# Kernel optimization log

Measured on AMD Instinct MI355X. Metric: run time of the kernel, lower is better.

## Reference

```python
import jax, jax.numpy as jnp
import numpy as np

NUM_HEADS = 8
NUM_GROUPS = 32  # min(C//4, 32) for C=512
EPS = 1e-6       # flax GroupNorm default


def setup_inputs() -> dict:
    key = jax.random.key(0)
    ks = jax.random.split(key, 3)
    B, H, W, D, C = 2, 16, 16, 16, 512
    x = jax.random.normal(ks[0], (B, H, W, D, C), dtype=jnp.float32)
    w_qkv = jax.random.normal(ks[1], (C, 3 * C), dtype=jnp.float32) / np.sqrt(C)
    w_proj = jax.random.normal(ks[2], (C, C), dtype=jnp.float32) / np.sqrt(C)
    return {
        "x": x,
        "gn_scale": jnp.ones((C,), jnp.float32),
        "gn_bias": jnp.zeros((C,), jnp.float32),
        "w_qkv": w_qkv,
        "b_qkv": jnp.zeros((3 * C,), jnp.float32),
        "w_proj": w_proj,
        "b_proj": jnp.zeros((C,), jnp.float32),
    }


def group_norm(x, scale, bias):
    # x: [B, S, C]; normalize within each of NUM_GROUPS channel groups over (S, group-channels)
    B, S, C = x.shape
    xg = x.reshape(B, S, NUM_GROUPS, C // NUM_GROUPS)
    mean = jnp.mean(xg, axis=(1, 3), keepdims=True)
    var = jnp.var(xg, axis=(1, 3), keepdims=True)
    xn = (xg - mean) * jax.lax.rsqrt(var + EPS)
    return xn.reshape(B, S, C) * scale + bias


def reference(x, gn_scale, gn_bias, w_qkv, b_qkv, w_proj, b_proj):
    B, H, W, D, C = x.shape
    S = H * W * D
    hd = C // NUM_HEADS
    xf = x.reshape(B, S, C)
    q_in = group_norm(xf, gn_scale, gn_bias)
    # 1x1x1 conv == per-position dense
    qkv = q_in @ w_qkv + b_qkv                      # [B, S, 3C]
    qkv = qkv.reshape(B, S, NUM_HEADS, 3 * hd)
    q, k, v = jnp.split(qkv, 3, axis=-1)            # each [B, S, nh, hd]
    scale = 1.0 / jnp.sqrt(jnp.asarray(hd, x.dtype))
    logits = jnp.einsum('btnh,bfnh->bnft', k, q * scale)  # [B, nh, S, S]
    weights = jax.nn.softmax(logits, axis=-1)
    h = jnp.einsum('bnft,btnh->bfnh', weights, v)   # [B, S, nh, hd]
    h = h.reshape(B, S, C) @ w_proj + b_proj
    return h.reshape(x.shape) + x
```

## Files before the change

kernel.cpp:

```cpp
#include <hip/hip_runtime.h>

typedef __attribute__((ext_vector_type(8))) short short8;
typedef __attribute__((ext_vector_type(4))) float f32x4;
typedef __attribute__((ext_vector_type(16))) float f32x16;

#define S_LEN 4096
#define C_DIM 512
#define NH 8
#define HD 64
#define NG 32
#define GS 16
#define LOG2E 1.44269504088896340736f

__device__ __forceinline__ unsigned short f2bf(float f) {
  union { float f; unsigned int u; } v; v.f = f;
  unsigned int r = v.u + 0x7fffu + ((v.u >> 16) & 1u);
  return (unsigned short)(r >> 16);
}

__device__ __forceinline__ float bf2f(unsigned short s) {
  union { unsigned u; float f; } v; v.u = (unsigned)s << 16;
  return v.f;
}

__device__ __forceinline__ float fexp2(float x) {
  float r;
  asm("v_exp_f32 %0, %1" : "=v"(r) : "v"(x));
  return r;
}

__device__ __forceinline__ unsigned pk_bf16(float a, float b) {
  unsigned r;
  asm("v_cvt_pk_bf16_f32 %0, %1, %2" : "=v"(r) : "v"(a), "v"(b));
  return r;
}

__device__ __forceinline__ void pl_swap(unsigned& a, unsigned& b) {
  asm("v_permlane32_swap_b32 %0, %1" : "+v"(a), "+v"(b));
}

__device__ __forceinline__ void gload_lds16(const void* g, void* l) {
  __builtin_amdgcn_global_load_lds((const __attribute__((address_space(1))) void*)g,
                                   (__attribute__((address_space(3))) void*)l, 16, 0, 0);
}

__global__ __launch_bounds__(256) void prep_kernel(const float* __restrict__ x,
                                                   float* __restrict__ partials,
                                                   const float* __restrict__ w_qkv,
                                                   unsigned short* __restrict__ wqkvT,
                                                   const float* __restrict__ w_proj,
                                                   unsigned short* __restrict__ wprojT) {
  __shared__ float tile[32][33];
  __shared__ float r1[4], r2[4];
  int bid = blockIdx.x;
  if (bid < 256) {
    int bg = bid >> 2, chunk = bid & 3;
    int b = bg >> 5, g = bg & 31;
    const float* xp = x + (size_t)b * S_LEN * C_DIM + g * GS;
    float s1 = 0.f, s2 = 0.f;
    for (int i = threadIdx.x; i < 1024 * 4; i += 256) {
      int s = chunk * 1024 + (i >> 2), c4 = i & 3;
      float4 v = *(const float4*)&xp[(size_t)s * C_DIM + c4 * 4];
      s1 += v.x + v.y + v.z + v.w;
      s2 += v.x * v.x + v.y * v.y + v.z * v.z + v.w * v.w;
    }
    for (int off = 1; off < 64; off <<= 1) {
      s1 += __shfl_xor(s1, off);
      s2 += __shfl_xor(s2, off);
    }
    int w = threadIdx.x >> 6;
    if ((threadIdx.x & 63) == 0) { r1[w] = s1; r2[w] = s2; }
    __syncthreads();
    if (threadIdx.x == 0) {
      partials[bg * 8 + chunk * 2]     = r1[0] + r1[1] + r1[2] + r1[3];
      partials[bg * 8 + chunk * 2 + 1] = r2[0] + r2[1] + r2[2] + r2[3];
    }
    return;
  }
  const float* src; unsigned short* dst; int K, N, n0, k0;
  if (bid < 1024) {
    int t = bid - 256;  src = w_qkv;  dst = wqkvT;  K = 512; N = 1536;
    n0 = (t % 48) * 32; k0 = (t / 48) * 32;
  } else {
    int t = bid - 1024; src = w_proj; dst = wprojT; K = 512; N = 512;
    n0 = (t % 16) * 32; k0 = (t / 16) * 32;
  }
  int c = threadIdx.x & 31, r0 = threadIdx.x >> 5;
  for (int i = 0; i < 4; ++i) {
    int r = r0 + i * 8;
    tile[r][c] = src[(size_t)(k0 + r) * N + n0 + c];
  }
  __syncthreads();
  for (int i = 0; i < 4; ++i) {
    int r = r0 + i * 8;
    dst[(size_t)(n0 + r) * K + k0 + c] = f2bf(tile[c][r]);
  }
}

__global__ __launch_bounds__(256) void gn_apply_kernel(const float* __restrict__ x,
                                                       const float* __restrict__ partials,
                                                       const float* __restrict__ scale,
                                                       const float* __restrict__ bias,
                                                       unsigned short* __restrict__ out) {
  int idx = blockIdx.x * 256 + threadIdx.x;
  int e = idx * 4;
  int c = e & (C_DIM - 1);
  int bs = e >> 9;
  int b = bs >> 12;
  int grp = b * NG + (c >> 4);
  float s1 = partials[grp * 8] + partials[grp * 8 + 2] + partials[grp * 8 + 4] + partials[grp * 8 + 6];
  float s2 = partials[grp * 8 + 1] + partials[grp * 8 + 3] + partials[grp * 8 + 5] + partials[grp * 8 + 7];
  const float invN = 1.0f / (float)(S_LEN * GS);
  float mean = s1 * invN;
  float var = s2 * invN - mean * mean;
  float rstd = rsqrtf(var + 1e-6f);
  float4 v = *(const float4*)&x[e];
  ushort4 o;
  o.x = f2bf((v.x - mean) * rstd * scale[c]     + bias[c]);
  o.y = f2bf((v.y - mean) * rstd * scale[c + 1] + bias[c + 1]);
  o.z = f2bf((v.z - mean) * rstd * scale[c + 2] + bias[c + 2]);
  o.w = f2bf((v.w - mean) * rstd * scale[c + 3] + bias[c + 3]);
  *(ushort4*)&out[e] = o;
}

template <int MODE>
__global__ __launch_bounds__(256) void gemm_kernel(const unsigned short* __restrict__ A,
                                                   const unsigned short* __restrict__ Bt,
                                                   const float* __restrict__ bias,
                                                   unsigned short* __restrict__ qh,
                                                   unsigned short* __restrict__ kh,
                                                   unsigned short* __restrict__ vh,
                                                   const float* __restrict__ resid,
                                                   float* __restrict__ outf) {
  __shared__ unsigned char Alds[16384];
  __shared__ unsigned char Blds[16384];
  int tid = threadIdx.x, lane = tid & 63, w = tid >> 6;
  int li = lane & 15, g = lane >> 4;
  int wr = (w >> 1) * 64, wc = (w & 1) * 64;
  int m0 = blockIdx.y * 128, n0 = blockIdx.x * 128;

  int srow = tid >> 3;
  int colS = (tid & 7) * 16;
  int sc   = colS ^ ((srow & 7) << 4);
  const char* aSrc = (const char*)A + (size_t)(m0 + srow) * 1024 + sc;
  const char* bSrc = (const char*)Bt + (size_t)(n0 + srow) * 1024 + sc;

  f32x4 acc[4][4];
  for (int i = 0; i < 4; ++i)
    for (int j = 0; j < 4; ++j) acc[i][j] = (f32x4){0.f, 0.f, 0.f, 0.f};

  for (int k0 = 0; k0 < 512; k0 += 64) {
#pragma unroll
    for (int r = 0; r < 4; ++r) {
      gload_lds16(aSrc + (size_t)r * 32 * 1024 + k0 * 2, &Alds[r * 4096 + tid * 16]);
      gload_lds16(bSrc + (size_t)r * 32 * 1024 + k0 * 2, &Blds[r * 4096 + tid * 16]);
    }
    asm volatile("s_waitcnt vmcnt(0)" ::: "memory");
    __builtin_amdgcn_s_barrier();

#pragma unroll
    for (int ks = 0; ks < 2; ++ks) {
      short8 af[4], bfm[4];
#pragma unroll
      for (int mi = 0; mi < 4; ++mi) {
        int row = wr + mi * 16 + li;
        af[mi] = *(const short8*)&Alds[row * 128 + ((ks * 64 + g * 16) ^ ((row & 7) << 4))];
      }
#pragma unroll
      for (int ni = 0; ni < 4; ++ni) {
        int row = wc + ni * 16 + li;
        bfm[ni] = *(const short8*)&Blds[row * 128 + ((ks * 64 + g * 16) ^ ((row & 7) << 4))];
      }
#pragma unroll
      for (int mi = 0; mi < 4; ++mi)
#pragma unroll
        for (int ni = 0; ni < 4; ++ni)
          acc[mi][ni] = __builtin_amdgcn_mfma_f32_16x16x32_bf16(af[mi], bfm[ni], acc[mi][ni], 0, 0, 0);
    }
    __syncthreads();
  }

  if (MODE == 0) {
    for (int ni = 0; ni < 4; ++ni) {
      int n = n0 + wc + ni * 16 + li;
      float bn = bias[n];
      int head = n / 192;
      int rem = n - head * 192;
      int part = rem >> 6;
      int h = rem & 63;
      unsigned short* dst = part == 0 ? qh : (part == 1 ? kh : vh);
      float mul = part == 0 ? 0.125f * LOG2E : 1.0f;
      for (int mi = 0; mi < 4; ++mi)
        for (int j = 0; j < 4; ++j) {
          int m = m0 + wr + mi * 16 + g * 4 + j;
          int b = m >> 12, s = m & 4095;
          float val = (acc[mi][ni][j] + bn) * mul;
          size_t idx;
          if (part == 2) idx = ((size_t)(b * NH + head) * HD + h) * S_LEN + s;
          else           idx = ((size_t)(b * NH + head) * S_LEN + s) * HD + h;
          dst[idx] = f2bf(val);
        }
    }
  } else {
    for (int ni = 0; ni < 4; ++ni) {
      int n = n0 + wc + ni * 16 + li;
      float bn = bias[n];
      for (int mi = 0; mi < 4; ++mi)
        for (int j = 0; j < 4; ++j) {
          int m = m0 + wr + mi * 16 + g * 4 + j;
          size_t off = (size_t)m * C_DIM + n;
          outf[off] = acc[mi][ni][j] + bn + resid[off];
        }
    }
  }
}

template <int SPLIT>
__global__ __launch_bounds__(256, 4) void attn_kernel(const unsigned short* __restrict__ qh,
                                                      const unsigned short* __restrict__ kh,
                                                      const unsigned short* __restrict__ vt,
                                                      unsigned short* __restrict__ ob,
                                                      unsigned short* __restrict__ opart,
                                                      float* __restrict__ lpart) {
  __shared__ unsigned char Kt[3 * 4096];
  __shared__ unsigned char Vt[3 * 4096];
  int bn = blockIdx.y;
  int half = SPLIT > 1 ? blockIdx.z : 0;
  int tid = threadIdx.x, lane = tid & 63, wv = tid >> 6;
  int r32 = lane & 31, hi_ = lane >> 5;
  int q0 = blockIdx.x * 128 + wv * 32;
  const int NT = S_LEN / 32 / SPLIT;
  const unsigned short* qp = qh + (size_t)bn * S_LEN * HD;
  const char* kp = (const char*)(kh + (size_t)bn * S_LEN * HD);
  const char* vp = (const char*)(vt + (size_t)bn * HD * S_LEN);

  int srow  = wv * 8 + (lane >> 3);
  int scolS = (lane & 7) * 16;
  int sc    = scolS ^ ((srow & 7) << 4);
  const char* kSrc = kp + (size_t)srow * 128 + sc + (size_t)half * (S_LEN / SPLIT) * 128;
  int vh_ = srow + ((sc >> 6) << 5);
  const char* vSrc = vp + (size_t)vh_ * (S_LEN * 2) + (sc & 63) + (size_t)half * (S_LEN / SPLIT) * 2;

  short8 qf[4];
#pragma unroll
  for (int ks = 0; ks < 4; ++ks)
    qf[ks] = *(const short8*)&qp[(size_t)(q0 + r32) * HD + ks * 16 + hi_ * 8];

  union { unsigned u[4]; short8 v; } ones;
#pragma unroll
  for (int i = 0; i < 4; ++i) ones.u[i] = 0x3F803F80u;

  f32x16 o0, o1, lacc, z16;
#pragma unroll
  for (int i = 0; i < 16; ++i) { o0[i] = 0.f; o1[i] = 0.f; lacc[i] = 0.f; z16[i] = 0.f; }

  int swzr = (r32 & 7) << 4;
  int sBase = wv * 1024;

  gload_lds16(kSrc, &Kt[sBase]);
  gload_lds16(vSrc, &Vt[sBase]);
  gload_lds16(kSrc + 32 * 128, &Kt[4096 + sBase]);
  gload_lds16(vSrc + 32 * 2,   &Vt[4096 + sBase]);
  asm volatile("s_waitcnt vmcnt(2)" ::: "memory");
  __builtin_amdgcn_s_barrier();

  int curO = 0, nxtO = 4096, nnO = 8192;
  for (int it = 0; it < NT; ++it) {
    bool more = (it + 2 < NT);
    if (more) {
      size_t t0n = (size_t)(it + 2) * 32;
      gload_lds16(kSrc + t0n * 128, &Kt[nnO + sBase]);
      gload_lds16(vSrc + t0n * 2,   &Vt[nnO + sBase]);
    }

    const unsigned char* Kr = &Kt[curO + r32 * 128];
    const unsigned char* Vr = &Vt[curO + r32 * 128];
    short8 kf[4], vf[4];
#pragma unroll
    for (int ks = 0; ks < 4; ++ks)
      kf[ks] = *(const short8*)&Kr[(ks * 32 + hi_ * 16) ^ swzr];
#pragma unroll
    for (int kk = 0; kk < 2; ++kk)
#pragma unroll
      for (int hf = 0; hf < 2; ++hf)
        vf[kk * 2 + hf] = *(const short8*)&Vr[(hf * 64 + kk * 32 + hi_ * 16) ^ swzr];

    f32x16 s = __builtin_amdgcn_mfma_f32_32x32x16_bf16(kf[0], qf[0], z16, 0, 0, 0);
#pragma unroll
    for (int ks = 1; ks < 4; ++ks)
      s = __builtin_amdgcn_mfma_f32_32x32x16_bf16(kf[ks], qf[ks], s, 0, 0, 0);

#pragma unroll
    for (int i = 0; i < 16; ++i) s[i] = fexp2(s[i]);

    unsigned pkv[8];
#pragma unroll
    for (int g2 = 0; g2 < 8; ++g2) pkv[g2] = pk_bf16(s[2 * g2], s[2 * g2 + 1]);
    pl_swap(pkv[0], pkv[2]); pl_swap(pkv[1], pkv[3]);
    pl_swap(pkv[4], pkv[6]); pl_swap(pkv[5], pkv[7]);
    union { unsigned u[4]; short8 v; } F0, F1;
    F0.u[0] = pkv[0]; F0.u[1] = pkv[1]; F0.u[2] = pkv[2]; F0.u[3] = pkv[3];
    F1.u[0] = pkv[4]; F1.u[1] = pkv[5]; F1.u[2] = pkv[6]; F1.u[3] = pkv[7];

    o0 = __builtin_amdgcn_mfma_f32_32x32x16_bf16(vf[0], F0.v, o0, 0, 0, 0);
    o1 = __builtin_amdgcn_mfma_f32_32x32x16_bf16(vf[1], F0.v, o1, 0, 0, 0);
    lacc = __builtin_amdgcn_mfma_f32_32x32x16_bf16(ones.v, F0.v, lacc, 0, 0, 0);
    o0 = __builtin_amdgcn_mfma_f32_32x32x16_bf16(vf[2], F1.v, o0, 0, 0, 0);
    o1 = __builtin_amdgcn_mfma_f32_32x32x16_bf16(vf[3], F1.v, o1, 0, 0, 0);
    lacc = __builtin_amdgcn_mfma_f32_32x32x16_bf16(ones.v, F1.v, lacc, 0, 0, 0);

    if (more) asm volatile("s_waitcnt vmcnt(2)" ::: "memory");
    else      asm volatile("s_waitcnt vmcnt(0)" ::: "memory");
    __builtin_amdgcn_s_barrier();
    int t = curO; curO = nxtO; nxtO = nnO; nnO = t;
  }

  if (SPLIT == 1) {
    float inv = 1.0f / lacc[0];
    int b = bn >> 3, n = bn & 7;
    size_t base = ((size_t)(b * S_LEN + q0 + r32)) * C_DIM + n * HD;
#pragma unroll
    for (int r = 0; r < 16; ++r) {
      int hrow = (r & 3) + 8 * (r >> 2) + 4 * hi_;
      ob[base + hrow]      = f2bf(o0[r] * inv);
      ob[base + 32 + hrow] = f2bf(o1[r] * inv);
    }
  } else {
    size_t row = (size_t)(bn * SPLIT + half) * S_LEN + q0 + r32;
    unsigned short* pp = opart + row * 64;
#pragma unroll
    for (int i = 0; i < 8; ++i) {
      int r = 2 * i;
      int hrow = (r & 3) + 8 * (r >> 2) + 4 * hi_;
      *(unsigned*)&pp[hrow]      = pk_bf16(o0[r], o0[r + 1]);
      *(unsigned*)&pp[32 + hrow] = pk_bf16(o1[r], o1[r + 1]);
    }
    if (!hi_) lpart[row] = lacc[0];
  }
}

template <int SPLIT>
__global__ __launch_bounds__(256) void attn_combine_kernel(const unsigned short* __restrict__ opart,
                                                           const float* __restrict__ lpart,
                                                           unsigned short* __restrict__ ob) {
  int idx = blockIdx.x * 256 + threadIdx.x;
  int h0 = (idx & 7) * 8;
  int q  = (idx >> 3) & (S_LEN - 1);
  int bn = idx >> 15;
  float acc[8];
#pragma unroll
  for (int j = 0; j < 8; ++j) acc[j] = 0.f;
  float lsum = 0.f;
#pragma unroll
  for (int z = 0; z < SPLIT; ++z) {
    size_t row = (size_t)(bn * SPLIT + z) * S_LEN + q;
    lsum += lpart[row];
    short8 a = *(const short8*)&opart[row * 64 + h0];
#pragma unroll
    for (int j = 0; j < 8; ++j) acc[j] += bf2f((unsigned short)a[j]);
  }
  float inv = 1.0f / lsum;
  union { unsigned short us[8]; short8 v; } R;
#pragma unroll
  for (int j = 0; j < 8; ++j) R.us[j] = f2bf(acc[j] * inv);
  int b_ = bn >> 3, n = bn & 7;
  *(short8*)&ob[((size_t)(b_ * S_LEN + q)) * C_DIM + n * HD + h0] = R.v;
}

extern "C" void kernel_launch(void* const* d_in, const int* in_sizes, int n_in,
                              void* d_out, int out_size, void* d_ws, size_t ws_size,
                              hipStream_t stream) {
  const float* x        = (const float*)d_in[0];
  const float* gn_scale = (const float*)d_in[1];
  const float* gn_bias  = (const float*)d_in[2];
  const float* w_qkv    = (const float*)d_in[3];
  const float* b_qkv    = (const float*)d_in[4];
  const float* w_proj   = (const float*)d_in[5];
  const float* b_proj   = (const float*)d_in[6];
  float* out = (float*)d_out;

  char* ws = (char*)d_ws;
  unsigned short* q_in   = (unsigned short*)(ws);
  unsigned short* wqkvT  = (unsigned short*)(ws + 8388608);
  unsigned short* wprojT = (unsigned short*)(ws + 9961472);
  unsigned short* qhb    = (unsigned short*)(ws + 10485760);
  unsigned short* khb    = (unsigned short*)(ws + 18874368);
  unsigned short* vtb    = (unsigned short*)(ws + 27262976);
  unsigned short* ahb    = (unsigned short*)(ws + 35651584);
  float* partials        = (float*)(ws + 44040192);
  float* lpart           = (float*)(ws + 44042240);
  unsigned short* opart  = (unsigned short*)(ws + 45090816);
  const size_t NEED2 = 45090816ull + (size_t)16 * 2 * S_LEN * 64 * 2;

  prep_kernel<<<1280, 256, 0, stream>>>(x, partials, w_qkv, wqkvT, w_proj, wprojT);
  gn_apply_kernel<<<4096, 256, 0, stream>>>(x, partials, gn_scale, gn_bias, q_in);
  gemm_kernel<0><<<dim3(12, 64), 256, 0, stream>>>(q_in, wqkvT, b_qkv, qhb, khb, vtb, nullptr, nullptr);
  if (ws_size >= NEED2) {
    attn_kernel<2><<<dim3(32, 16, 2), 256, 0, stream>>>(qhb, khb, vtb, ahb, opart, lpart);
    attn_combine_kernel<2><<<2048, 256, 0, stream>>>(opart, lpart, ahb);
  } else {
    attn_kernel<1><<<dim3(32, 16, 1), 256, 0, stream>>>(qhb, khb, vtb, ahb, nullptr, nullptr);
  }
  gemm_kernel<1><<<dim3(4, 64), 256, 0, stream>>>(ahb, wprojT, b_proj, nullptr, nullptr, nullptr, x, out);
}
```

Measured before the change: 153.5 us.

## Fuse split-KV attention combine into output projection GEMM; vectorize V stores

Removes the separate attention-combine kernel. The output projection GEMM now reads the two bf16 split partials and the row sums directly, normalizes and sums them while staging the A tile into LDS, then runs the MFMA GEMM with the bias and residual epilogue. This drops one launch and one round trip of the attention output through global memory. It also packs the transposed V writes in the QKV GEMM epilogue into 4-wide ushort4 stores. In exchange, each projection block recomputes the combine for its A rows, and across the four N-tile blocks that is four times the combine reads and math.

After: 151.5 us. About the same (-1.3%).

```diff
diff --git a/kernel.cpp b/kernel.cpp
--- a/kernel.cpp
+++ b/kernel.cpp
@@ -188,18 +188,28 @@
       int rem = n - head * 192;
       int part = rem >> 6;
       int h = rem & 63;
-      unsigned short* dst = part == 0 ? qh : (part == 1 ? kh : vh);
-      float mul = part == 0 ? 0.125f * LOG2E : 1.0f;
-      for (int mi = 0; mi < 4; ++mi)
-        for (int j = 0; j < 4; ++j) {
-          int m = m0 + wr + mi * 16 + g * 4 + j;
+      if (part == 2) {
+        for (int mi = 0; mi < 4; ++mi) {
+          int m = m0 + wr + mi * 16 + g * 4;
           int b = m >> 12, s = m & 4095;
-          float val = (acc[mi][ni][j] + bn) * mul;
-          size_t idx;
-          if (part == 2) idx = ((size_t)(b * NH + head) * HD + h) * S_LEN + s;
-          else           idx = ((size_t)(b * NH + head) * S_LEN + s) * HD + h;
-          dst[idx] = f2bf(val);
+          size_t idx = ((size_t)(b * NH + head) * HD + h) * S_LEN + s;
+          ushort4 val;
+          val.x = f2bf(acc[mi][ni][0] + bn);
+          val.y = f2bf(acc[mi][ni][1] + bn);
+          val.z = f2bf(acc[mi][ni][2] + bn);
+          val.w = f2bf(acc[mi][ni][3] + bn);
+          *(ushort4*)&vh[idx] = val;
         }
+      } else {
+        unsigned short* dst = part == 0 ? qh : kh;
+        float mul = part == 0 ? 0.125f * LOG2E : 1.0f;
+        for (int mi = 0; mi < 4; ++mi)
+          for (int j = 0; j < 4; ++j) {
+            int m = m0 + wr + mi * 16 + g * 4 + j;
+            int b = m >> 12, s = m & 4095;
+            dst[((size_t)(b * NH + head) * S_LEN + s) * HD + h] = f2bf((acc[mi][ni][j] + bn) * mul);
+          }
+      }
     }
   } else {
     for (int ni = 0; ni < 4; ++ni) {
@@ -212,6 +222,103 @@
           outf[off] = acc[mi][ni][j] + bn + resid[off];
         }
     }
+  }
+}
+
+__global__ __launch_bounds__(256) void gemm_proj_kernel(const unsigned short* __restrict__ opart,
+                                                        const float* __restrict__ lpart,
+                                                        const unsigned short* __restrict__ Bt,
+                                                        const float* __restrict__ bias,
+                                                        const float* __restrict__ resid,
+                                                        float* __restrict__ outf) {
+  __shared__ unsigned char Alds[16384];
+  __shared__ unsigned char Blds[16384];
+  __shared__ float linv[8][128];
+  int tid = threadIdx.x, lane = tid & 63, w = tid >> 6;
+  int li = lane & 15, g = lane >> 4;
+  int wr = (w >> 1) * 64, wc = (w & 1) * 64;
+  int m0 = blockIdx.y * 128, n0 = blockIdx.x * 128;
+  int b_ = m0 >> 12;
+  int s0 = m0 & 4095;
+
+  int srow = tid >> 3;
+  int colS = (tid & 7) * 16;
+  int sc   = colS ^ ((srow & 7) << 4);
+  const char* bSrc = (const char*)Bt + (size_t)(n0 + srow) * 1024 + sc;
+
+#pragma unroll
+  for (int i = 0; i < 4; ++i) {
+    int e = tid + i * 256;
+    int hd_ = e >> 7, r = e & 127;
+    size_t rowA = (size_t)((b_ * NH + hd_) * 2) * S_LEN + s0 + r;
+    linv[hd_][r] = 1.0f / (lpart[rowA] + lpart[rowA + S_LEN]);
+  }
+  __syncthreads();
+
+  int tr = tid >> 1, hf2 = tid & 1;
+  size_t rowBase = ((size_t)(b_ * NH) * 2) * S_LEN + s0 + tr;
+
+  f32x4 acc[4][4];
+  for (int i = 0; i < 4; ++i)
+    for (int j = 0; j < 4; ++j) acc[i][j] = (f32x4){0.f, 0.f, 0.f, 0.f};
+
+  for (int k0 = 0; k0 < 512; k0 += 64) {
+    int head = k0 >> 6;
+#pragma unroll
+    for (int r = 0; r < 4; ++r)
+      gload_lds16(bSrc + (size_t)r * 32 * 1024 + k0 * 2, &Blds[r * 4096 + tid * 16]);
+
+    size_t rowA = rowBase + (size_t)head * 2 * S_LEN;
+    const unsigned short* pA0 = opart + rowA * 64 + hf2 * 32;
+    const unsigned short* pA1 = opart + (rowA + S_LEN) * 64 + hf2 * 32;
+    float inv = linv[head][tr];
+#pragma unroll
+    for (int q = 0; q < 4; ++q) {
+      short8 x = *(const short8*)&pA0[q * 8];
+      short8 y = *(const short8*)&pA1[q * 8];
+      union { unsigned u[4]; short8 v; } d;
+#pragma unroll
+      for (int p = 0; p < 4; ++p) {
+        float f0 = (bf2f((unsigned short)x[2 * p])     + bf2f((unsigned short)y[2 * p]))     * inv;
+        float f1 = (bf2f((unsigned short)x[2 * p + 1]) + bf2f((unsigned short)y[2 * p + 1])) * inv;
+        d.u[p] = pk_bf16(f0, f1);
+      }
+      int cc = hf2 * 64 + q * 16;
+      *(short8*)&Alds[tr * 128 + (cc ^ ((tr & 7) << 4))] = d.v;
+    }
+    __syncthreads();
+
+#pragma unroll
+    for (int ks = 0; ks < 2; ++ks) {
+      short8 af[4], bfm[4];
+#pragma unroll
+      for (int mi = 0; mi < 4; ++mi) {
+        int row = wr + mi * 16 + li;
+        af[mi] = *(const short8*)&Alds[row * 128 + ((ks * 64 + g * 16) ^ ((row & 7) << 4))];
+      }
+#pragma unroll
+      for (int ni = 0; ni < 4; ++ni) {
+        int row = wc + ni * 16 + li;
+        bfm[ni] = *(const short8*)&Blds[row * 128 + ((ks * 64 + g * 16) ^ ((row & 7) << 4))];
+      }
+#pragma unroll
+      for (int mi = 0; mi < 4; ++mi)
+#pragma unroll
+        for (int ni = 0; ni < 4; ++ni)
+          acc[mi][ni] = __builtin_amdgcn_mfma_f32_16x16x32_bf16(af[mi], bfm[ni], acc[mi][ni], 0, 0, 0);
+    }
+    __syncthreads();
+  }
+
+  for (int ni = 0; ni < 4; ++ni) {
+    int n = n0 + wc + ni * 16 + li;
+    float bn = bias[n];
+    for (int mi = 0; mi < 4; ++mi)
+      for (int j = 0; j < 4; ++j) {
+        int m = m0 + wr + mi * 16 + g * 4 + j;
+        size_t off = (size_t)m * C_DIM + n;
+        outf[off] = acc[mi][ni][j] + bn + resid[off];
+      }
   }
 }
 
@@ -339,34 +446,6 @@
   }
 }
 
-template <int SPLIT>
-__global__ __launch_bounds__(256) void attn_combine_kernel(const unsigned short* __restrict__ opart,
-                                                           const float* __restrict__ lpart,
-                                                           unsigned short* __restrict__ ob) {
-  int idx = blockIdx.x * 256 + threadIdx.x;
-  int h0 = (idx & 7) * 8;
-  int q  = (idx >> 3) & (S_LEN - 1);
-  int bn = idx >> 15;
-  float acc[8];
-#pragma unroll
-  for (int j = 0; j < 8; ++j) acc[j] = 0.f;
-  float lsum = 0.f;
-#pragma unroll
-  for (int z = 0; z < SPLIT; ++z) {
-    size_t row = (size_t)(bn * SPLIT + z) * S_LEN + q;
-    lsum += lpart[row];
-    short8 a = *(const short8*)&opart[row * 64 + h0];
-#pragma unroll
-    for (int j = 0; j < 8; ++j) acc[j] += bf2f((unsigned short)a[j]);
-  }
-  float inv = 1.0f / lsum;
-  union { unsigned short us[8]; short8 v; } R;
-#pragma unroll
-  for (int j = 0; j < 8; ++j) R.us[j] = f2bf(acc[j] * inv);
-  int b_ = bn >> 3, n = bn & 7;
-  *(short8*)&ob[((size_t)(b_ * S_LEN + q)) * C_DIM + n * HD + h0] = R.v;
-}
-
 extern "C" void kernel_launch(void* const* d_in, const int* in_sizes, int n_in,
                               void* d_out, int out_size, void* d_ws, size_t ws_size,
                               hipStream_t stream) {
@@ -396,10 +475,10 @@
   gn_apply_kernel<<<4096, 256, 0, stream>>>(x, partials, gn_scale, gn_bias, q_in);
   gemm_kernel<0><<<dim3(12, 64), 256, 0, stream>>>(q_in, wqkvT, b_qkv, qhb, khb, vtb, nullptr, nullptr);
   if (ws_size >= NEED2) {
-    attn_kernel<2><<<dim3(32, 16, 2), 256, 0, stream>>>(qhb, khb, vtb, ahb, opart, lpart);
-    attn_combine_kernel<2><<<2048, 256, 0, stream>>>(opart, lpart, ahb);
+    attn_kernel<2><<<dim3(32, 16, 2), 256, 0, stream>>>(qhb, khb, vtb, nullptr, opart, lpart);
+    gemm_proj_kernel<<<dim3(4, 64), 256, 0, stream>>>(opart, lpart, wprojT, b_proj, x, out);
   } else {
     attn_kernel<1><<<dim3(32, 16, 1), 256, 0, stream>>>(qhb, khb, vtb, ahb, nullptr, nullptr);
-  }
-  gemm_kernel<1><<<dim3(4, 64), 256, 0, stream>>>(ahb, wprojT, b_proj, nullptr, nullptr, nullptr, x, out);
-}
+    gemm_kernel<1><<<dim3(4, 64), 256, 0, stream>>>(ahb, wprojT, b_proj, nullptr, nullptr, nullptr, x, out);
+  }
+}
```
